# Kernel optimization log

Measured on AMD Instinct MI355X. Metric: run time of the kernel, lower is better.

The kernel has to match this reference:

```python
import jax, jax.numpy as jnp
import numpy as np

N, D = 16384, 1024
M, K = 64, 256          # num_subvecs, num_clusters
d = D // M              # elements per subvector


def setup_inputs() -> dict:
    key = jax.random.key(0)
    k1, k2 = jax.random.split(key)
    embeds = jax.random.normal(k1, (N, D), dtype=jnp.float32)
    codebooks = jax.random.normal(k2, (M, K, d), dtype=jnp.float32)  # per-subvector KMeans centroids
    return {"embeds": embeds, "codebooks": codebooks}


def reference(embeds, codebooks):
    # to_indices: per-subvector squared-L2 nearest centroid, then from_indices gather.
    n, dim = embeds.shape
    m, k, sub = codebooks.shape
    x = embeds.reshape(n, m, sub)                       # [N, M, d] subvector view
    x2 = jnp.sum(x * x, axis=-1)[..., None]             # [N, M, 1]
    c2 = jnp.sum(codebooks * codebooks, axis=-1)[None]  # [1, M, K]
    xc = jnp.einsum('nmd,mkd->nmk', x, codebooks)       # [N, M, K]
    dists = x2 - 2.0 * xc + c2                          # squared L2 ||x - c||^2
    idx = jnp.argmin(dists, axis=-1)                    # [N, M] PQ codes
    # from_indices: gather assigned codewords and concatenate per embedding
    recon = codebooks[jnp.arange(m)[None, :], idx]      # [N, M, d]
    return recon.reshape(n, dim)                        # [N, D]
```

## Files before the change

### kernel.cpp

```cpp
#include <hip/hip_runtime.h>


#define DIMS   1024
#define MSUB   64
#define KCODE  256
#define DSUB   16
#define FLCAP  128

static constexpr float MARGIN = 2e-3f;

typedef __attribute__((ext_vector_type(8))) short s16x8;
typedef __attribute__((ext_vector_type(4))) float f32x4;
typedef __attribute__((ext_vector_type(4))) unsigned int u32x4;

static __device__ __forceinline__ f32x4 mfma32(s16x8 a, s16x8 b, f32x4 c) {
    return __builtin_amdgcn_mfma_f32_16x16x32_bf16(a, b, c, 0, 0, 0);
}

static __device__ __forceinline__ void mk_bfrags(float4 xv, s16x8& B1, s16x8& B2) {
    unsigned u0 = __float_as_uint(xv.x), u1 = __float_as_uint(xv.y);
    unsigned u2 = __float_as_uint(xv.z), u3 = __float_as_uint(xv.w);
    unsigned h01 = (u1 & 0xFFFF0000u) | (u0 >> 16);
    unsigned h23 = (u3 & 0xFFFF0000u) | (u2 >> 16);
    float l0 = xv.x - __uint_as_float(u0 & 0xFFFF0000u);
    float l1 = xv.y - __uint_as_float(u1 & 0xFFFF0000u);
    float l2 = xv.z - __uint_as_float(u2 & 0xFFFF0000u);
    float l3 = xv.w - __uint_as_float(u3 & 0xFFFF0000u);
    unsigned l01 = (__float_as_uint(l1) & 0xFFFF0000u) | (__float_as_uint(l0) >> 16);
    unsigned l23 = (__float_as_uint(l3) & 0xFFFF0000u) | (__float_as_uint(l2) >> 16);
    B1 = __builtin_bit_cast(s16x8, (u32x4){h01, h23, h01, h23});
    B2 = __builtin_bit_cast(s16x8, (u32x4){l01, l23, l01, l23});
}

__global__ __launch_bounds__(256, 2) void pq_main(
    const float* __restrict__ embeds,
    const float* __restrict__ codebooks,
    float* __restrict__ out,
    unsigned* __restrict__ flag_cnt,
    unsigned* __restrict__ flag_list,
    unsigned flag_cap)
{
    __shared__ u32x4 chcl[16 * 64];
    __shared__ float cnorm[KCODE];
    __shared__ unsigned fl_buf[FLCAP];
    __shared__ unsigned fl_cnt, fl_base;

    const int tid = threadIdx.x;
    const int bid = blockIdx.x;
    const int m   = (bid >> 3) & 63;
    const int g   = (bid & 7) | ((bid >> 9) << 3);
    const float* cbm = codebooks + (size_t)m * (KCODE * DSUB);

    if (tid == 0) fl_cnt = 0;

    {
        const float4* src = (const float4*)(cbm + tid * DSUB);
        float c[16];
        #pragma unroll
        for (int q = 0; q < 4; ++q) {
            float4 v = src[q];
            c[4*q+0] = v.x; c[4*q+1] = v.y; c[4*q+2] = v.z; c[4*q+3] = v.w;
        }
        float ss = 0.f;
        #pragma unroll
        for (int j = 0; j < 16; ++j) ss = fmaf(c[j], c[j], ss);
        cnorm[tid] = -0.5f * ss;
        #pragma unroll
        for (int d = 0; d < 4; ++d) {
            unsigned uc0 = __float_as_uint(c[4*d+0]), uc1 = __float_as_uint(c[4*d+1]);
            unsigned uc2 = __float_as_uint(c[4*d+2]), uc3 = __float_as_uint(c[4*d+3]);
            unsigned hc01 = (uc1 & 0xFFFF0000u) | (uc0 >> 16);
            unsigned hc23 = (uc3 & 0xFFFF0000u) | (uc2 >> 16);
            float lc0 = c[4*d+0] - __uint_as_float(uc0 & 0xFFFF0000u);
            float lc1 = c[4*d+1] - __uint_as_float(uc1 & 0xFFFF0000u);
            float lc2 = c[4*d+2] - __uint_as_float(uc2 & 0xFFFF0000u);
            float lc3 = c[4*d+3] - __uint_as_float(uc3 & 0xFFFF0000u);
            unsigned lc01 = (__float_as_uint(lc1) & 0xFFFF0000u) | (__float_as_uint(lc0) >> 16);
            unsigned lc23 = (__float_as_uint(lc3) & 0xFFFF0000u) | (__float_as_uint(lc2) >> 16);
            chcl[(tid >> 4) * 64 + d * 16 + (tid & 15)] = (u32x4){hc01, hc23, lc01, lc23};
        }
    }
    __syncthreads();

    const int w   = tid >> 6;
    const int l   = tid & 63;
    const int col = l & 15;
    const int ds  = l >> 4;
    const int n0  = (g << 9) + (w << 7);

    const float* xp = embeds + (size_t)(n0 + col) * DIMS + m * DSUB + ds * 4;
    float*       op = out    + (size_t)(n0 + col) * DIMS + m * DSUB + ds * 4;
    const u32x4* av  = chcl + l;
    const f32x4* hvp = (const f32x4*)cnorm + ds;
    const unsigned MSK = 0xFFFFFF00u;
    const size_t RS = 16 * DIMS;

    float4 xv0 = *(const float4*)(xp);
    float4 xv1 = *(const float4*)(xp + RS);
    float4 xv2 = *(const float4*)(xp + 2 * RS);
    float4 xv3 = *(const float4*)(xp + 3 * RS);

    #pragma unroll 1
    for (int p = 0; p < 2; ++p) {
        s16x8 B1_0, B2_0, B1_1, B2_1, B1_2, B2_2, B1_3, B2_3;
        mk_bfrags(xv0, B1_0, B2_0);
        mk_bfrags(xv1, B1_1, B2_1);
        mk_bfrags(xv2, B1_2, B2_2);
        mk_bfrags(xv3, B1_3, B2_3);
        if (p == 0) {
            xv0 = *(const float4*)(xp + 4 * RS);
            xv1 = *(const float4*)(xp + 5 * RS);
            xv2 = *(const float4*)(xp + 6 * RS);
            xv3 = *(const float4*)(xp + 7 * RS);
        }

        float b0 = -3e38f, s0 = -3e38f, b1 = -3e38f, s1 = -3e38f;
        float b2 = -3e38f, s2 = -3e38f, b3 = -3e38f, s3 = -3e38f;

        #pragma unroll
        for (int kt = 0; kt < 16; ++kt) {
            s16x8 A = __builtin_bit_cast(s16x8, av[kt * 64]);
            f32x4 h = hvp[kt * 4];
            f32x4 a0 = mfma32(A, B1_0, h); a0 = mfma32(A, B2_0, a0);
            f32x4 a1 = mfma32(A, B1_1, h); a1 = mfma32(A, B2_1, a1);
            f32x4 a2 = mfma32(A, B1_2, h); a2 = mfma32(A, B2_2, a2);
            f32x4 a3 = mfma32(A, B1_3, h); a3 = mfma32(A, B2_3, a3);
            #pragma unroll
            for (int r = 0; r < 4; ++r) {
                const unsigned code = (unsigned)(kt * 16 + r);
                float p0 = __uint_as_float((__float_as_uint(a0[r]) & MSK) | code);
                s0 = fmaxf(s0, fminf(p0, b0)); b0 = fmaxf(b0, p0);
                float p1 = __uint_as_float((__float_as_uint(a1[r]) & MSK) | code);
                s1 = fmaxf(s1, fminf(p1, b1)); b1 = fmaxf(b1, p1);
                float p2 = __uint_as_float((__float_as_uint(a2[r]) & MSK) | code);
                s2 = fmaxf(s2, fminf(p2, b2)); b2 = fmaxf(b2, p2);
                float p3 = __uint_as_float((__float_as_uint(a3[r]) & MSK) | code);
                s3 = fmaxf(s3, fminf(p3, b3)); b3 = fmaxf(b3, p3);
            }
        }

        const unsigned d4 = (unsigned)(ds * 4);
        b0 = __uint_as_float(__float_as_uint(b0) + d4);
        s0 = __uint_as_float(__float_as_uint(s0) + d4);
        b1 = __uint_as_float(__float_as_uint(b1) + d4);
        s1 = __uint_as_float(__float_as_uint(s1) + d4);
        b2 = __uint_as_float(__float_as_uint(b2) + d4);
        s2 = __uint_as_float(__float_as_uint(s2) + d4);
        b3 = __uint_as_float(__float_as_uint(b3) + d4);
        s3 = __uint_as_float(__float_as_uint(s3) + d4);

        #pragma unroll
        for (int msk = 16; msk <= 32; msk <<= 1) {
            float o;
            o = __shfl_xor(b0, msk); float q0 = __shfl_xor(s0, msk);
            s0 = fmaxf(fmaxf(s0, q0), fminf(b0, o)); b0 = fmaxf(b0, o);
            o = __shfl_xor(b1, msk); float q1 = __shfl_xor(s1, msk);
            s1 = fmaxf(fmaxf(s1, q1), fminf(b1, o)); b1 = fmaxf(b1, o);
            o = __shfl_xor(b2, msk); float q2 = __shfl_xor(s2, msk);
            s2 = fmaxf(fmaxf(s2, q2), fminf(b2, o)); b2 = fmaxf(b2, o);
            o = __shfl_xor(b3, msk); float q3 = __shfl_xor(s3, msk);
            s3 = fmaxf(fmaxf(s3, q3), fminf(b3, o)); b3 = fmaxf(b3, o);
        }

        const int i0 = (int)(__float_as_uint(b0) & 255u);
        const int i1 = (int)(__float_as_uint(b1) & 255u);
        const int i2 = (int)(__float_as_uint(b2) & 255u);
        const int i3 = (int)(__float_as_uint(b3) & 255u);

        float* obase = op + (size_t)p * 4 * RS;
        *(float4*)(obase)          = *(const float4*)(cbm + (size_t)i0 * DSUB + ds * 4);
        *(float4*)(obase + RS)     = *(const float4*)(cbm + (size_t)i1 * DSUB + ds * 4);
        *(float4*)(obase + 2 * RS) = *(const float4*)(cbm + (size_t)i2 * DSUB + ds * 4);
        *(float4*)(obase + 3 * RS) = *(const float4*)(cbm + (size_t)i3 * DSUB + ds * 4);

        if (ds == 0) {
            const int nb = n0 + p * 64 + col;
            float bb[4] = {b0, b1, b2, b3}, sb[4] = {s0, s1, s2, s3};
            #pragma unroll
            for (int s = 0; s < 4; ++s) {
                float gap = __uint_as_float(__float_as_uint(bb[s]) & MSK) -
                            __uint_as_float(__float_as_uint(sb[s]) & MSK);
                if (gap < MARGIN) {
                    unsigned ent = (unsigned)((nb + s * 16) * 64 + m);
                    unsigned q = atomicAdd(&fl_cnt, 1u);
                    if (q < FLCAP) fl_buf[q] = ent;
                    else { unsigned qq = atomicAdd(flag_cnt, 1u);
                           if (qq < flag_cap) flag_list[qq] = ent; }
                }
            }
        }
    }

    __syncthreads();
    unsigned c = fl_cnt; if (c > FLCAP) c = FLCAP;
    if (tid == 0) fl_base = atomicAdd(flag_cnt, c);
    __syncthreads();
    const unsigned base = fl_base;
    for (unsigned i = tid; i < c; i += 256) {
        unsigned q = base + i;
        if (q < flag_cap) flag_list[q] = fl_buf[i];
    }
}

__global__ __launch_bounds__(256) void pq_refine(
    const float* __restrict__ embeds,
    const float* __restrict__ codebooks,
    float* __restrict__ out,
    const unsigned* __restrict__ flag_cnt,
    const unsigned* __restrict__ flag_list,
    unsigned flag_cap)
{
    unsigned cnt = *flag_cnt;
    if (cnt > flag_cap) cnt = flag_cap;
    const int l = threadIdx.x & 63;
    const unsigned wid = (blockIdx.x << 2) | (unsigned)(threadIdx.x >> 6);
    const unsigned nw  = gridDim.x << 2;

    for (unsigned i = wid; i < cnt; i += nw) {
        const unsigned e = flag_list[i];
        const int n = (int)(e >> 6), m = (int)(e & 63u);
        const float* xrow = embeds + (size_t)n * DIMS + m * DSUB;
        double xd[DSUB];
        #pragma unroll
        for (int dd = 0; dd < DSUB; ++dd) xd[dd] = (double)xrow[dd];
        const float* cbm = codebooks + (size_t)m * (KCODE * DSUB);

        double bd = 1e300;
        int bi = 0;
        #pragma unroll 1
        for (int cc = 0; cc < 4; ++cc) {
            const int c = l * 4 + cc;
            const float* cp = cbm + c * DSUB;
            double s = 0.0;
            #pragma unroll
            for (int dd = 0; dd < DSUB; ++dd) {
                double diff = xd[dd] - (double)cp[dd];
                s = fma(diff, diff, s);
            }
            if (s < bd) { bd = s; bi = c; }
        }
        #pragma unroll
        for (int msk = 1; msk <= 32; msk <<= 1) {
            double ob = __shfl_xor(bd, msk);
            int   oi  = __shfl_xor(bi, msk);
            if (ob < bd || (ob == bd && oi < bi)) { bd = ob; bi = oi; }
        }
        if (l < DSUB) out[(size_t)n * DIMS + m * DSUB + l] = cbm[bi * DSUB + l];
    }
}

extern "C" void kernel_launch(void* const* d_in, const int* in_sizes, int n_in,
                              void* d_out, int out_size, void* d_ws, size_t ws_size,
                              hipStream_t stream)
{
    const float* embeds    = (const float*)d_in[0];
    const float* codebooks = (const float*)d_in[1];
    float* out = (float*)d_out;

    unsigned* flag_cnt  = (unsigned*)d_ws;
    unsigned* flag_list = (unsigned*)d_ws + 4;
    unsigned flag_cap = 0;
    if (ws_size >= 32) {
        size_t cap = (ws_size - 16) / sizeof(unsigned);
        flag_cap = (cap > 0x7FFFFFFFull) ? 0x7FFFFFFFu : (unsigned)cap;
    }

    hipMemsetAsync(d_ws, 0, 16, stream);

    pq_main<<<dim3(2048), dim3(256), 0, stream>>>(
        embeds, codebooks, out, flag_cnt, flag_list, flag_cap);

    pq_refine<<<dim3(256), dim3(256), 0, stream>>>(
        embeds, codebooks, out, flag_cnt, flag_list, flag_cap);
}
```

Before: 90.82 us.

## Write PQ codes as bytes, refine codes, then gather codewords in separate pass

The main kernel no longer writes float4 codewords. It stores a one-byte code per (row, subvector) in the first bytes of each output row, which serves as scratch. Refinement fixes the flagged codes in place, and a new gather kernel reads the codes and writes full codeword rows with coalesced row-wise stores. This removes scattered 16-byte writes and the duplicate writes from refinement, at the cost of an extra kernel launch and an extra read of the byte codes. The flag detection also now spreads across all lanes instead of only ds==0 lanes.

Result: slower. 93.49 us (+2.9%).

```diff
diff --git a/kernel.cpp b/kernel.cpp
--- a/kernel.cpp
+++ b/kernel.cpp
@@ -35,7 +35,7 @@
 __global__ __launch_bounds__(256, 2) void pq_main(
     const float* __restrict__ embeds,
     const float* __restrict__ codebooks,
-    float* __restrict__ out,
+    unsigned char* __restrict__ outb,
     unsigned* __restrict__ flag_cnt,
     unsigned* __restrict__ flag_list,
     unsigned flag_cap)
@@ -89,7 +89,6 @@
     const int n0  = (g << 9) + (w << 7);
 
     const float* xp = embeds + (size_t)(n0 + col) * DIMS + m * DSUB + ds * 4;
-    float*       op = out    + (size_t)(n0 + col) * DIMS + m * DSUB + ds * 4;
     const u32x4* av  = chcl + l;
     const f32x4* hvp = (const f32x4*)cnorm + ds;
     const unsigned MSK = 0xFFFFFF00u;
@@ -162,32 +161,19 @@
             s3 = fmaxf(fmaxf(s3, q3), fminf(b3, o)); b3 = fmaxf(b3, o);
         }
 
-        const int i0 = (int)(__float_as_uint(b0) & 255u);
-        const int i1 = (int)(__float_as_uint(b1) & 255u);
-        const int i2 = (int)(__float_as_uint(b2) & 255u);
-        const int i3 = (int)(__float_as_uint(b3) & 255u);
-
-        float* obase = op + (size_t)p * 4 * RS;
-        *(float4*)(obase)          = *(const float4*)(cbm + (size_t)i0 * DSUB + ds * 4);
-        *(float4*)(obase + RS)     = *(const float4*)(cbm + (size_t)i1 * DSUB + ds * 4);
-        *(float4*)(obase + 2 * RS) = *(const float4*)(cbm + (size_t)i2 * DSUB + ds * 4);
-        *(float4*)(obase + 3 * RS) = *(const float4*)(cbm + (size_t)i3 * DSUB + ds * 4);
-
-        if (ds == 0) {
-            const int nb = n0 + p * 64 + col;
-            float bb[4] = {b0, b1, b2, b3}, sb[4] = {s0, s1, s2, s3};
-            #pragma unroll
-            for (int s = 0; s < 4; ++s) {
-                float gap = __uint_as_float(__float_as_uint(bb[s]) & MSK) -
-                            __uint_as_float(__float_as_uint(sb[s]) & MSK);
-                if (gap < MARGIN) {
-                    unsigned ent = (unsigned)((nb + s * 16) * 64 + m);
-                    unsigned q = atomicAdd(&fl_cnt, 1u);
-                    if (q < FLCAP) fl_buf[q] = ent;
-                    else { unsigned qq = atomicAdd(flag_cnt, 1u);
-                           if (qq < flag_cap) flag_list[qq] = ent; }
-                }
-            }
+        float bs_ = (l & 32) ? ((l & 16) ? b3 : b2) : ((l & 16) ? b1 : b0);
+        float ss_ = (l & 32) ? ((l & 16) ? s3 : s2) : ((l & 16) ? s1 : s0);
+        const int row = n0 + p * 64 + l;
+        outb[(size_t)row * (DIMS * 4) + m] = (unsigned char)(__float_as_uint(bs_) & 255u);
+
+        float gap = __uint_as_float(__float_as_uint(bs_) & MSK) -
+                    __uint_as_float(__float_as_uint(ss_) & MSK);
+        if (gap < MARGIN) {
+            unsigned ent = (unsigned)(row * 64 + m);
+            unsigned q = atomicAdd(&fl_cnt, 1u);
+            if (q < FLCAP) fl_buf[q] = ent;
+            else { unsigned qq = atomicAdd(flag_cnt, 1u);
+                   if (qq < flag_cap) flag_list[qq] = ent; }
         }
     }
 
@@ -205,7 +191,7 @@
 __global__ __launch_bounds__(256) void pq_refine(
     const float* __restrict__ embeds,
     const float* __restrict__ codebooks,
-    float* __restrict__ out,
+    unsigned char* __restrict__ outb,
     const unsigned* __restrict__ flag_cnt,
     const unsigned* __restrict__ flag_list,
     unsigned flag_cap)
@@ -245,7 +231,31 @@
             int   oi  = __shfl_xor(bi, msk);
             if (ob < bd || (ob == bd && oi < bi)) { bd = ob; bi = oi; }
         }
-        if (l < DSUB) out[(size_t)n * DIMS + m * DSUB + l] = cbm[bi * DSUB + l];
+        if (l == 0) outb[(size_t)n * (DIMS * 4) + m] = (unsigned char)bi;
+    }
+}
+
+__global__ __launch_bounds__(256) void pq_gather(
+    const float* __restrict__ codebooks,
+    float* __restrict__ out)
+{
+    const unsigned char* outb = (const unsigned char*)out;
+    const int tid = threadIdx.x;
+    const int m   = tid >> 2;
+    const int seg = tid & 3;
+    const int n0  = blockIdx.x * 8;
+
+    unsigned char ids[8];
+    #pragma unroll
+    for (int r = 0; r < 8; ++r)
+        ids[r] = outb[(size_t)(n0 + r) * (DIMS * 4) + m];
+    __syncthreads();
+
+    #pragma unroll
+    for (int r = 0; r < 8; ++r) {
+        const float4 v = *(const float4*)(codebooks +
+                          ((size_t)m * KCODE + ids[r]) * DSUB + seg * 4);
+        *(float4*)(out + (size_t)(n0 + r) * DIMS + tid * 4) = v;
     }
 }
 
@@ -268,8 +278,10 @@
     hipMemsetAsync(d_ws, 0, 16, stream);
 
     pq_main<<<dim3(2048), dim3(256), 0, stream>>>(
-        embeds, codebooks, out, flag_cnt, flag_list, flag_cap);
+        embeds, codebooks, (unsigned char*)d_out, flag_cnt, flag_list, flag_cap);
 
     pq_refine<<<dim3(256), dim3(256), 0, stream>>>(
-        embeds, codebooks, out, flag_cnt, flag_list, flag_cap);
-}
+        embeds, codebooks, (unsigned char*)d_out, flag_cnt, flag_list, flag_cap);
+
+    pq_gather<<<dim3(2048), dim3(256), 0, stream>>>(codebooks, out);
+}
```
